# Performance work log

Hardware: AMD Instinct MI355X
Metric: run time of the kernel (lower is better)

The kernel has to match this reference:

```python
import jax, jax.numpy as jnp
import numpy as np

DIM = 384
NUM_HEADS = 12
HEAD_DIM = DIM // NUM_HEADS  # 32
SCALE = HEAD_DIM ** -0.5
B, N = 4, 2048


def setup_inputs() -> dict:
    key = jax.random.key(0)
    k0, k1, k2, k3 = jax.random.split(key, 4)
    x = jax.random.normal(k0, (B, N, DIM), dtype=jnp.float32)
    # nn.Linear(dim, 3*dim, bias=False): y = x @ W_qkv, W_qkv is [C, 3C]
    W_qkv = jax.random.normal(k1, (DIM, 3 * DIM), dtype=jnp.float32) * (DIM ** -0.5)
    # nn.Linear(dim, dim): y = x @ W_proj + b_proj, W_proj is [C, C]
    W_proj = jax.random.normal(k2, (DIM, DIM), dtype=jnp.float32) * (DIM ** -0.5)
    b_proj = jax.random.normal(k3, (DIM,), dtype=jnp.float32) * 0.01
    return {"x": x, "W_qkv": W_qkv, "W_proj": W_proj, "b_proj": b_proj}


def reference(x, W_qkv, W_proj, b_proj):
    b, n, c = x.shape
    qkv = (x @ W_qkv).reshape(b, n, 3, NUM_HEADS, HEAD_DIM)
    qkv = jnp.transpose(qkv, (2, 0, 3, 1, 4))  # [3, B, H, N, hd]
    q, k, v = qkv[0], qkv[1], qkv[2]
    # full attention: softmax(q k^T * scale) v
    attn = jnp.einsum('bhqd,bhkd->bhqk', q, k) * SCALE  # [B,H,N,N]
    attn = jax.nn.softmax(attn, axis=-1)
    out = jnp.einsum('bhqk,bhkd->bhqd', attn, v)  # [B,H,N,hd]
    out = jnp.transpose(out, (0, 2, 1, 3)).reshape(b, n, c)
    return out @ W_proj + b_proj
```

## Files before the change

kernel.cpp:

```cpp
#include <hip/hip_runtime.h>

constexpr int BB  = 4;
constexpr int SEQ = 2048;
constexpr int CC  = 384;
constexpr int C3  = 1152;
constexpr int NH  = 12;
constexpr int HD  = 32;
constexpr float SCALE = 0.17677669529663689f;
constexpr float LOG2E = 1.4426950408889634f;
constexpr float KSC   = SCALE * LOG2E;
constexpr size_t KV_BYTES = (size_t)2 * BB * NH * SEQ * HD * 2;
constexpr size_t WT_BYTES = ((size_t)C3 * CC + (size_t)CC * CC) * 2;
constexpr size_t XB_BYTES = (size_t)BB * SEQ * CC * 2;

typedef __attribute__((ext_vector_type(8))) short short8_t;
typedef __attribute__((ext_vector_type(4))) float floatx4;

#if __has_builtin(__builtin_amdgcn_exp2f)
#define EXP2F __builtin_amdgcn_exp2f
#else
#define EXP2F __builtin_exp2f
#endif

__device__ __forceinline__ unsigned short f2bf(float f) {
    unsigned int u = __builtin_bit_cast(unsigned int, f);
    u += 0x7fffu + ((u >> 16) & 1u);
    return (unsigned short)(u >> 16);
}
__device__ __forceinline__ unsigned int pk_rn(float lo, float hi) {
    return __builtin_amdgcn_perm(__builtin_bit_cast(unsigned int, hi) + 0x8000u,
                                 __builtin_bit_cast(unsigned int, lo) + 0x8000u,
                                 0x07060302u);
}
__device__ __forceinline__ unsigned int cvtpk(float lo, float hi) {
    unsigned int r;
    asm("v_cvt_pk_bf16_f32 %0, %1, %2" : "=v"(r) : "v"(lo), "v"(hi));
    return r;
}
__device__ __forceinline__ short8_t pack8(float4 a, float4 b) {
    uint4 u;
    u.x = pk_rn(a.x, a.y); u.y = pk_rn(a.z, a.w);
    u.z = pk_rn(b.x, b.y); u.w = pk_rn(b.z, b.w);
    return __builtin_bit_cast(short8_t, u);
}

__device__ __forceinline__ void vstore(unsigned short* vb, short8_t a, short8_t b) {
    const uint4 ua = __builtin_bit_cast(uint4, a);
    const uint4 ub = __builtin_bit_cast(uint4, b);
    *(uint2*)(vb)      = (uint2){ua.x, ua.y};
    *(uint2*)(vb + 8)  = (uint2){ua.z, ua.w};
    *(uint2*)(vb + 16) = (uint2){ub.x, ub.y};
    *(uint2*)(vb + 24) = (uint2){ub.z, ub.w};
}

__global__ __launch_bounds__(256) void prep_kernel(
    const float* __restrict__ x, const float* __restrict__ wqkv,
    const float* __restrict__ wproj,
    unsigned short* __restrict__ wqkvT, unsigned short* __restrict__ wprojT,
    unsigned short* __restrict__ xb)
{
    const int bid = blockIdx.x;
    if (bid >= 144) {
        const size_t base = (size_t)(bid - 144) * 2048 + threadIdx.x * 8;
        const float4 a = *(const float4*)(x + base);
        const float4 b = *(const float4*)(x + base + 4);
        uint4 u;
        u.x = pk_rn(a.x, a.y); u.y = pk_rn(a.z, a.w);
        u.z = pk_rn(b.x, b.y); u.w = pk_rn(b.z, b.w);
        *(uint4*)(xb + base) = u;
        return;
    }
    __shared__ float ls[64][68];
    const float* src; unsigned short* dst; int SN, k0, n0;
    if (bid < 108) {
        src = wqkv; dst = wqkvT; SN = C3;
        k0 = (bid / 18) * 64; n0 = (bid % 18) * 64;
    } else {
        const int b2 = bid - 108;
        src = wproj; dst = wprojT; SN = CC;
        k0 = (b2 / 6) * 64; n0 = (b2 % 6) * 64;
    }
    const int t  = threadIdx.x;
    const int rr = t >> 4, cc4 = (t & 15) * 4;
#pragma unroll
    for (int p = 0; p < 4; ++p) {
        const int row = p * 16 + rr;
        const float4 v = *(const float4*)&src[(size_t)(k0 + row) * SN + n0 + cc4];
        ls[row][cc4] = v.x; ls[row][cc4 + 1] = v.y;
        ls[row][cc4 + 2] = v.z; ls[row][cc4 + 3] = v.w;
    }
    __syncthreads();
#pragma unroll
    for (int p = 0; p < 4; ++p) {
        const int nrow = p * 16 + rr;
        uint2 u;
        u.x = pk_rn(ls[cc4][nrow],     ls[cc4 + 1][nrow]);
        u.y = pk_rn(ls[cc4 + 2][nrow], ls[cc4 + 3][nrow]);
        *(uint2*)&dst[(size_t)(n0 + nrow) * CC + k0 + cc4] = u;
    }
}

__global__ __launch_bounds__(256) void qkv_fast(
    const unsigned short* __restrict__ xb,
    const unsigned short* __restrict__ wT,
    unsigned short* __restrict__ qb,
    unsigned short* __restrict__ kv)
{
    __shared__ __align__(16) unsigned short As[2][128][40];
    __shared__ __align__(16) unsigned short Bs[2][128][40];

    const int mt   = blockIdx.x & 63;
    const int nb   = blockIdx.x >> 6;
    const int tid  = threadIdx.x;
    const int wid  = tid >> 6;
    const int lane = tid & 63;
    const int quad = lane >> 4;
    const int col  = lane & 15;
    const int wr   = wid >> 1, wc = wid & 1;
    const int m0 = mt * 128, n0 = nb * 128;

    const int arow = tid >> 1;
    const int aoff = (tid & 1) * 16;

    floatx4 acc[4][4];
#pragma unroll
    for (int i = 0; i < 4; ++i)
#pragma unroll
        for (int j = 0; j < 4; ++j) acc[i][j] = (floatx4){0.f, 0.f, 0.f, 0.f};

    const unsigned short* xrow = xb + (size_t)(m0 + arow) * CC + aoff;
    const unsigned short* wrow = wT + (size_t)(n0 + arow) * CC + aoff;

    short8_t ast0, ast1, bst0, bst1;
    ast0 = *(const short8_t*)xrow;
    ast1 = *(const short8_t*)(xrow + 8);
    bst0 = *(const short8_t*)wrow;
    bst1 = *(const short8_t*)(wrow + 8);
    *(short8_t*)&As[0][arow][aoff]     = ast0;
    *(short8_t*)&As[0][arow][aoff + 8] = ast1;
    *(short8_t*)&Bs[0][arow][aoff]     = bst0;
    *(short8_t*)&Bs[0][arow][aoff + 8] = bst1;

    for (int it = 0; it < CC / 32; ++it) {
        const int kn = (it + 1 < CC / 32) ? (it + 1) * 32 : 0;
        ast0 = *(const short8_t*)(xrow + kn);
        ast1 = *(const short8_t*)(xrow + kn + 8);
        bst0 = *(const short8_t*)(wrow + kn);
        bst1 = *(const short8_t*)(wrow + kn + 8);

        __syncthreads();
        const int p = it & 1;
        short8_t af[4], bf[4];
#pragma unroll
        for (int i = 0; i < 4; ++i)
            af[i] = *(const short8_t*)&As[p][wr * 64 + i * 16 + col][quad * 8];
#pragma unroll
        for (int j = 0; j < 4; ++j)
            bf[j] = *(const short8_t*)&Bs[p][wc * 64 + j * 16 + col][quad * 8];
#pragma unroll
        for (int j = 0; j < 4; ++j)
#pragma unroll
            for (int i = 0; i < 4; ++i)
                acc[i][j] = __builtin_amdgcn_mfma_f32_16x16x32_bf16(af[i], bf[j], acc[i][j], 0, 0, 0);

        *(short8_t*)&As[p ^ 1][arow][aoff]     = ast0;
        *(short8_t*)&As[p ^ 1][arow][aoff + 8] = ast1;
        *(short8_t*)&Bs[p ^ 1][arow][aoff]     = bst0;
        *(short8_t*)&Bs[p ^ 1][arow][aoff + 8] = bst1;
    }

    const int t = nb / 3;
#pragma unroll
    for (int i = 0; i < 4; ++i) {
        const int mg = m0 + wr * 64 + i * 16 + quad * 4;
        if (t == 0) {
#pragma unroll
            for (int j = 0; j < 4; ++j) {
                const int n = n0 + wc * 64 + j * 16 + col;
#pragma unroll
                for (int r = 0; r < 4; ++r)
                    qb[(size_t)(mg + r) * CC + n] = f2bf(acc[i][j][r]);
            }
        } else if (t == 1) {
            const int b = mg >> 11, s = mg & (SEQ - 1);
#pragma unroll
            for (int j = 0; j < 4; ++j) {
                const int rem = n0 - CC + wc * 64 + j * 16 + col;
                const int h = rem >> 5, d = rem & 31;
                unsigned short* kp = kv + ((size_t)(b * NH + h) * SEQ + s) * HD + d;
#pragma unroll
                for (int r = 0; r < 4; ++r)
                    kp[(size_t)r * HD] = f2bf(acc[i][j][r] * KSC);
            }
        } else {
            const int b = mg >> 11, s = mg & (SEQ - 1);
            unsigned short* vtb = kv + (size_t)BB * NH * SEQ * HD;
#pragma unroll
            for (int j = 0; j < 4; ++j) {
                const int rem = n0 - 2 * CC + wc * 64 + j * 16 + col;
                const int h = rem >> 5, d = rem & 31;
                uint2 u;
                u.x = pk_rn(acc[i][j][0], acc[i][j][1]);
                u.y = pk_rn(acc[i][j][2], acc[i][j][3]);
                *(uint2*)&vtb[((size_t)(b * NH + h) * HD + d) * SEQ + s] = u;
            }
        }
    }
}

__global__ __launch_bounds__(256, 3) void attn_kernel(
    const unsigned short* __restrict__ kv,
    const unsigned short* __restrict__ qb,
    unsigned short* __restrict__ ab)
{
    const int bid  = blockIdx.x;
    const int qp   = bid / 48;
    const int bh   = bid % 48;
    const int h    = bh % NH;
    const int b    = bh / NH;
    const int w    = threadIdx.x >> 6;
    const int lane = threadIdx.x & 63;
    const int quad = lane >> 4;
    const int col  = lane & 15;
    const int tid  = threadIdx.x;

    const unsigned short* K  = kv + (size_t)bh * SEQ * HD;
    const unsigned short* VT = kv + (size_t)BB * NH * SEQ * HD + (size_t)bh * HD * SEQ;

    __shared__ __align__(16) unsigned short Vt[2][32][136];

    const int drow_s = tid >> 3, voff_s = (tid & 7) * 16;
    const int vbase  = ((tid & 6) >> 1) * 32 + (tid & 1) * 4;

    const unsigned short* Kf = K + (size_t)col * HD + quad * 8;

    int qrow[2];
    short8_t qf[2];
#pragma unroll
    for (int t = 0; t < 2; ++t) {
        qrow[t] = b * SEQ + qp * 128 + (w + 4 * t) * 16 + col;
        qf[t] = *(const short8_t*)(qb + (size_t)qrow[t] * CC + h * HD + quad * 8);
    }

    short8_t ones;
#pragma unroll
    for (int e = 0; e < 8; ++e) ones[e] = (short)0x3F80;

    floatx4 o[2][2];
    floatx4 lacc[2];
#pragma unroll
    for (int t = 0; t < 2; ++t) {
        lacc[t] = (floatx4){0.f, 0.f, 0.f, 0.f};
#pragma unroll
        for (int i = 0; i < 2; ++i) o[t][i] = (floatx4){0.f, 0.f, 0.f, 0.f};
    }
    const float ci = -10.f * LOG2E;
    const floatx4 cinit = {ci, ci, ci, ci};

    short8_t v0a = *(const short8_t*)(VT + (size_t)drow_s * SEQ + voff_s);
    short8_t v0b = *(const short8_t*)(VT + (size_t)drow_s * SEQ + voff_s + 8);
    vstore(&Vt[0][drow_s][vbase], v0a, v0b);

    short8_t kaf[4][2];
#pragma unroll
    for (int c = 0; c < 4; ++c) {
        kaf[c][0] = *(const short8_t*)(Kf + (size_t)(c * 32) * HD);
        kaf[c][1] = *(const short8_t*)(Kf + (size_t)(c * 32 + 16) * HD);
    }

    for (int it = 0; it < SEQ / 128; ++it) {
        const int kn = ((it + 1) * 128) & (SEQ - 1);
        v0a = *(const short8_t*)(VT + (size_t)drow_s * SEQ + kn + voff_s);
        v0b = *(const short8_t*)(VT + (size_t)drow_s * SEQ + kn + voff_s + 8);
        const unsigned short* Kn = Kf + (size_t)kn * HD;

        __syncthreads();
        const int p = it & 1;

        short8_t va[4][2];
#pragma unroll
        for (int c = 0; c < 4; ++c) {
            const int c32 = c * 32;
            va[c][0] = *(const short8_t*)&Vt[p][col][c32 + quad * 8];
            va[c][1] = *(const short8_t*)&Vt[p][16 + col][c32 + quad * 8];
        }

#pragma unroll
        for (int c = 0; c < 4; ++c) {
            floatx4 s0[2], s1[2];
            __builtin_amdgcn_s_setprio(1);
#pragma unroll
            for (int t = 0; t < 2; ++t) {
                s0[t] = __builtin_amdgcn_mfma_f32_16x16x32_bf16(kaf[c][0], qf[t], cinit, 0, 0, 0);
                s1[t] = __builtin_amdgcn_mfma_f32_16x16x32_bf16(kaf[c][1], qf[t], cinit, 0, 0, 0);
            }
            __builtin_amdgcn_s_setprio(0);
            kaf[c][0] = *(const short8_t*)(Kn + (size_t)(c * 32) * HD);
            kaf[c][1] = *(const short8_t*)(Kn + (size_t)(c * 32 + 16) * HD);

            short8_t pb[2];
#pragma unroll
            for (int t = 0; t < 2; ++t) {
                const float p00 = EXP2F(s0[t][0]), p01 = EXP2F(s0[t][1]);
                const float p02 = EXP2F(s0[t][2]), p03 = EXP2F(s0[t][3]);
                const float p10 = EXP2F(s1[t][0]), p11 = EXP2F(s1[t][1]);
                const float p12 = EXP2F(s1[t][2]), p13 = EXP2F(s1[t][3]);
                const uint4 pu = {cvtpk(p00, p01), cvtpk(p02, p03),
                                  cvtpk(p10, p11), cvtpk(p12, p13)};
                pb[t] = __builtin_bit_cast(short8_t, pu);
            }
            __builtin_amdgcn_s_setprio(1);
#pragma unroll
            for (int t = 0; t < 2; ++t) {
                o[t][0] = __builtin_amdgcn_mfma_f32_16x16x32_bf16(va[c][0], pb[t], o[t][0], 0, 0, 0);
                o[t][1] = __builtin_amdgcn_mfma_f32_16x16x32_bf16(va[c][1], pb[t], o[t][1], 0, 0, 0);
                lacc[t] = __builtin_amdgcn_mfma_f32_16x16x32_bf16(ones, pb[t], lacc[t], 0, 0, 0);
            }
            __builtin_amdgcn_s_setprio(0);
        }

        vstore(&Vt[p ^ 1][drow_s][vbase], v0a, v0b);
    }

#pragma unroll
    for (int t = 0; t < 2; ++t) {
        const float inv = 1.f / lacc[t][0];
        unsigned short* op = ab + (size_t)qrow[t] * CC + h * HD;
#pragma unroll
        for (int i = 0; i < 2; ++i) {
            uint2 u;
            u.x = pk_rn(o[t][i][0] * inv, o[t][i][1] * inv);
            u.y = pk_rn(o[t][i][2] * inv, o[t][i][3] * inv);
            *(uint2*)&op[i * 16 + quad * 4] = u;
        }
    }
}

__global__ __launch_bounds__(256) void proj_fast(
    const unsigned short* __restrict__ ab,
    const unsigned short* __restrict__ wT,
    const float* __restrict__ bias,
    float* __restrict__ out)
{
    __shared__ __align__(16) unsigned short Bs[2][384][32];

    const int mt   = blockIdx.x;
    const int tid  = threadIdx.x;
    const int wid  = tid >> 6;
    const int lane = tid & 63;
    const int quad = lane >> 4;
    const int col  = lane & 15;
    const int m0   = mt * 32;

    floatx4 acc[2][6];
#pragma unroll
    for (int i = 0; i < 2; ++i)
#pragma unroll
        for (int j = 0; j < 6; ++j) acc[i][j] = (floatx4){0.f, 0.f, 0.f, 0.f};

    const unsigned short* arow0 = ab + (size_t)(m0 + col) * CC + quad * 8;
    const unsigned short* arow1 = arow0 + (size_t)16 * CC;

    short8_t bst[3][2];
    short8_t af0, af1;
    {
#pragma unroll
        for (int j = 0; j < 3; ++j) {
            const int f = j * 256 + tid;
            const unsigned short* wp = wT + (size_t)(f >> 1) * CC + (f & 1) * 16;
            bst[j][0] = *(const short8_t*)wp;
            bst[j][1] = *(const short8_t*)(wp + 8);
        }
        af0 = *(const short8_t*)arow0;
        af1 = *(const short8_t*)arow1;
#pragma unroll
        for (int j = 0; j < 3; ++j) {
            const int f = j * 256 + tid;
            *(short8_t*)&Bs[0][f >> 1][(f & 1) * 16]     = bst[j][0];
            *(short8_t*)&Bs[0][f >> 1][(f & 1) * 16 + 8] = bst[j][1];
        }
    }

    for (int it = 0; it < CC / 32; ++it) {
        const int kn = (it + 1 < CC / 32) ? (it + 1) * 32 : 0;
#pragma unroll
        for (int j = 0; j < 3; ++j) {
            const int f = j * 256 + tid;
            const unsigned short* wp = wT + (size_t)(f >> 1) * CC + kn + (f & 1) * 16;
            bst[j][0] = *(const short8_t*)wp;
            bst[j][1] = *(const short8_t*)(wp + 8);
        }
        const short8_t afn0 = *(const short8_t*)(arow0 + kn);
        const short8_t afn1 = *(const short8_t*)(arow1 + kn);

        __syncthreads();
        const int p = it & 1;
        short8_t bf[6];
#pragma unroll
        for (int j = 0; j < 6; ++j)
            bf[j] = *(const short8_t*)&Bs[p][wid * 96 + j * 16 + col][quad * 8];
#pragma unroll
        for (int j = 0; j < 6; ++j) {
            acc[0][j] = __builtin_amdgcn_mfma_f32_16x16x32_bf16(af0, bf[j], acc[0][j], 0, 0, 0);
            acc[1][j] = __builtin_amdgcn_mfma_f32_16x16x32_bf16(af1, bf[j], acc[1][j], 0, 0, 0);
        }

#pragma unroll
        for (int j = 0; j < 3; ++j) {
            const int f = j * 256 + tid;
            *(short8_t*)&Bs[p ^ 1][f >> 1][(f & 1) * 16]     = bst[j][0];
            *(short8_t*)&Bs[p ^ 1][f >> 1][(f & 1) * 16 + 8] = bst[j][1];
        }
        af0 = afn0; af1 = afn1;
    }

#pragma unroll
    for (int j = 0; j < 6; ++j) {
        const int n = wid * 96 + j * 16 + col;
        const float bv = bias[n];
#pragma unroll
        for (int i = 0; i < 2; ++i)
#pragma unroll
            for (int r = 0; r < 4; ++r)
                out[(size_t)(m0 + i * 16 + quad * 4 + r) * CC + n] = acc[i][j][r] + bv;
    }
}

__global__ __launch_bounds__(256) void qkv_lds(
    const float* __restrict__ x, const float* __restrict__ w,
    float* __restrict__ dq, unsigned short* __restrict__ kv)
{
    __shared__ __align__(16) unsigned short wt[128 * 40];
    const int mt = blockIdx.x & 63, nb = blockIdx.x >> 6;
    const int tid = threadIdx.x, wid = tid >> 6, lane = tid & 63;
    const int quad = lane >> 4, col = lane & 15;
    const int wr = wid >> 1, wc = wid & 1;
    const int m0 = mt * 128, n0 = nb * 128;
    const int sn = tid >> 1, skg = (tid & 1) * 4;

    floatx4 acc[4][4];
#pragma unroll
    for (int i = 0; i < 4; ++i)
#pragma unroll
        for (int j = 0; j < 4; ++j) acc[i][j] = (floatx4){0.f, 0.f, 0.f, 0.f};
    const float* xbase = x + (size_t)(m0 + wr * 64 + col) * CC;

    for (int kb = 0; kb < CC; kb += 32) {
        float wv[4][4];
#pragma unroll
        for (int s = 0; s < 4; ++s) {
            const int k = kb + (skg + s) * 4;
#pragma unroll
            for (int j = 0; j < 4; ++j) wv[s][j] = w[(size_t)(k + j) * C3 + n0 + sn];
        }
        short8_t af[4];
#pragma unroll
        for (int i = 0; i < 4; ++i) {
            const float* xr = xbase + (size_t)i * 16 * CC + kb + quad * 8;
            af[i] = pack8(*(const float4*)xr, *(const float4*)(xr + 4));
        }
        __syncthreads();
#pragma unroll
        for (int s = 0; s < 4; ++s) {
            ushort4 u;
            u.x = f2bf(wv[s][0]); u.y = f2bf(wv[s][1]);
            u.z = f2bf(wv[s][2]); u.w = f2bf(wv[s][3]);
            *(ushort4*)&wt[sn * 40 + (skg + s) * 4] = u;
        }
        __syncthreads();
#pragma unroll
        for (int j = 0; j < 4; ++j) {
            const short8_t bf = *(const short8_t*)&wt[(wc * 64 + j * 16 + col) * 40 + quad * 8];
#pragma unroll
            for (int i = 0; i < 4; ++i)
                acc[i][j] = __builtin_amdgcn_mfma_f32_16x16x32_bf16(af[i], bf, acc[i][j], 0, 0, 0);
        }
    }
    const int t = nb / 3;
#pragma unroll
    for (int i = 0; i < 4; ++i) {
        const int mg = m0 + wr * 64 + i * 16 + quad * 4;
        if (t == 0) {
#pragma unroll
            for (int j = 0; j < 4; ++j) {
                const int n = n0 + wc * 64 + j * 16 + col;
#pragma unroll
                for (int r = 0; r < 4; ++r) dq[(size_t)(mg + r) * CC + n] = acc[i][j][r];
            }
        } else if (t == 1) {
            const int b = mg >> 11, s = mg & (SEQ - 1);
#pragma unroll
            for (int j = 0; j < 4; ++j) {
                const int rem = n0 - CC + wc * 64 + j * 16 + col;
                const int h = rem >> 5, d = rem & 31;
                unsigned short* kp = kv + ((size_t)(b * NH + h) * SEQ + s) * HD + d;
#pragma unroll
                for (int r = 0; r < 4; ++r) kp[(size_t)r * HD] = f2bf(acc[i][j][r]);
            }
        } else {
            const int b = mg >> 11, s = mg & (SEQ - 1);
            unsigned short* vtb = kv + (size_t)BB * NH * SEQ * HD;
#pragma unroll
            for (int j = 0; j < 4; ++j) {
                const int rem = n0 - 2 * CC + wc * 64 + j * 16 + col;
                const int h = rem >> 5, d = rem & 31;
                uint2 u;
                u.x = pk_rn(acc[i][j][0], acc[i][j][1]);
                u.y = pk_rn(acc[i][j][2], acc[i][j][3]);
                *(uint2*)&vtb[((size_t)(b * NH + h) * HD + d) * SEQ + s] = u;
            }
        }
    }
}

__global__ __launch_bounds__(256) void attn_f32(
    const unsigned short* __restrict__ kv,
    float* qatt)
{
    const int bid  = blockIdx.x;
    const int qp   = bid / 48;
    const int bh   = bid % 48;
    const int h    = bh % NH;
    const int b    = bh / NH;
    const int w    = threadIdx.x >> 6;
    const int lane = threadIdx.x & 63;
    const int quad = lane >> 4;
    const int col  = lane & 15;
    const int tid  = threadIdx.x;

    const unsigned short* K  = kv + (size_t)bh * SEQ * HD;
    const unsigned short* VT = kv + (size_t)BB * NH * SEQ * HD + (size_t)bh * HD * SEQ;

    __shared__ __align__(16) unsigned short Kt[2][128][40];
    __shared__ __align__(16) unsigned short Vt[2][32][136];

    const int krow_s = tid >> 1, koff_s = (tid & 1) * 16;
    const int drow_s = tid >> 3, voff_s = (tid & 7) * 16;

    int qrow[2];
    short8_t qf[2];
    const float sc = SCALE * LOG2E;
#pragma unroll
    for (int t = 0; t < 2; ++t) {
        qrow[t] = b * SEQ + qp * 128 + (w + 4 * t) * 16 + col;
        const float* qpt = qatt + (size_t)qrow[t] * CC + h * HD + quad * 8;
        const float4 a0 = *(const float4*)qpt;
        const float4 a1 = *(const float4*)(qpt + 4);
        const float4 s0 = {a0.x * sc, a0.y * sc, a0.z * sc, a0.w * sc};
        const float4 s1 = {a1.x * sc, a1.y * sc, a1.z * sc, a1.w * sc};
        qf[t] = pack8(s0, s1);
    }

    short8_t ones;
#pragma unroll
    for (int e = 0; e < 8; ++e) ones[e] = (short)0x3F80;

    floatx4 o[2][2];
    floatx4 lacc[2];
#pragma unroll
    for (int t = 0; t < 2; ++t) {
        lacc[t] = (floatx4){0.f, 0.f, 0.f, 0.f};
#pragma unroll
        for (int i = 0; i < 2; ++i) o[t][i] = (floatx4){0.f, 0.f, 0.f, 0.f};
    }
    const float ci = -10.f * LOG2E;
    const floatx4 cinit = {ci, ci, ci, ci};

    short8_t k0a = *(const short8_t*)(K + (size_t)krow_s * HD + koff_s);
    short8_t k0b = *(const short8_t*)(K + (size_t)krow_s * HD + koff_s + 8);
    short8_t v0a = *(const short8_t*)(VT + (size_t)drow_s * SEQ + voff_s);
    short8_t v0b = *(const short8_t*)(VT + (size_t)drow_s * SEQ + voff_s + 8);
    *(short8_t*)&Kt[0][krow_s][koff_s]     = k0a;
    *(short8_t*)&Kt[0][krow_s][koff_s + 8] = k0b;
    *(short8_t*)&Vt[0][drow_s][voff_s]     = v0a;
    *(short8_t*)&Vt[0][drow_s][voff_s + 8] = v0b;

    for (int it = 0; it < SEQ / 128; ++it) {
        const int kn = ((it + 1) * 128) & (SEQ - 1);
        k0a = *(const short8_t*)(K + (size_t)(kn + krow_s) * HD + koff_s);
        k0b = *(const short8_t*)(K + (size_t)(kn + krow_s) * HD + koff_s + 8);
        v0a = *(const short8_t*)(VT + (size_t)drow_s * SEQ + kn + voff_s);
        v0b = *(const short8_t*)(VT + (size_t)drow_s * SEQ + kn + voff_s + 8);

        __syncthreads();
        const int p = it & 1;

#pragma unroll
        for (int c = 0; c < 4; ++c) {
            const int c32 = c * 32;
            const short8_t ka0 = *(const short8_t*)&Kt[p][c32 + col][quad * 8];
            const short8_t ka1 = *(const short8_t*)&Kt[p][c32 + 16 + col][quad * 8];
            const uint2 w0a = *(const uint2*)&Vt[p][col][c32 + quad * 4];
            const uint2 w0b = *(const uint2*)&Vt[p][col][c32 + 16 + quad * 4];
            const uint2 w1a = *(const uint2*)&Vt[p][16 + col][c32 + quad * 4];
            const uint2 w1b = *(const uint2*)&Vt[p][16 + col][c32 + 16 + quad * 4];
            const short8_t va0 = __builtin_bit_cast(short8_t, (uint4){w0a.x, w0a.y, w0b.x, w0b.y});
            const short8_t va1 = __builtin_bit_cast(short8_t, (uint4){w1a.x, w1a.y, w1b.x, w1b.y});
#pragma unroll
            for (int t = 0; t < 2; ++t) {
                const floatx4 s0 = __builtin_amdgcn_mfma_f32_16x16x32_bf16(ka0, qf[t], cinit, 0, 0, 0);
                const floatx4 s1 = __builtin_amdgcn_mfma_f32_16x16x32_bf16(ka1, qf[t], cinit, 0, 0, 0);
                const float p00 = EXP2F(s0[0]), p01 = EXP2F(s0[1]);
                const float p02 = EXP2F(s0[2]), p03 = EXP2F(s0[3]);
                const float p10 = EXP2F(s1[0]), p11 = EXP2F(s1[1]);
                const float p12 = EXP2F(s1[2]), p13 = EXP2F(s1[3]);
                const uint4 pu = {pk_rn(p00, p01), pk_rn(p02, p03),
                                  pk_rn(p10, p11), pk_rn(p12, p13)};
                const short8_t pb = __builtin_bit_cast(short8_t, pu);
                o[t][0] = __builtin_amdgcn_mfma_f32_16x16x32_bf16(va0, pb, o[t][0], 0, 0, 0);
                o[t][1] = __builtin_amdgcn_mfma_f32_16x16x32_bf16(va1, pb, o[t][1], 0, 0, 0);
                lacc[t] = __builtin_amdgcn_mfma_f32_16x16x32_bf16(ones, pb, lacc[t], 0, 0, 0);
            }
        }

        *(short8_t*)&Kt[p ^ 1][krow_s][koff_s]     = k0a;
        *(short8_t*)&Kt[p ^ 1][krow_s][koff_s + 8] = k0b;
        *(short8_t*)&Vt[p ^ 1][drow_s][voff_s]     = v0a;
        *(short8_t*)&Vt[p ^ 1][drow_s][voff_s + 8] = v0b;
    }

#pragma unroll
    for (int t = 0; t < 2; ++t) {
        const float inv = 1.f / lacc[t][0];
        float* op = qatt + (size_t)qrow[t] * CC + h * HD;
#pragma unroll
        for (int r = 0; r < 4; ++r) {
            op[quad * 4 + r]      = o[t][0][r] * inv;
            op[16 + quad * 4 + r] = o[t][1][r] * inv;
        }
    }
}

__global__ __launch_bounds__(256) void proj_lds(
    float* att, const float* __restrict__ wp, const float* __restrict__ bias)
{
    __shared__ __align__(16) unsigned short wt[CC * 40];
    const int mt = blockIdx.x, tid = threadIdx.x, wid = tid >> 6, lane = tid & 63;
    const int quad = lane >> 4, col = lane & 15;
    const int m0 = mt * 16;
    floatx4 acc[6];
#pragma unroll
    for (int j = 0; j < 6; ++j) acc[j] = (floatx4){0.f, 0.f, 0.f, 0.f};
    for (int kb = 0; kb < CC; kb += 32) {
        float gv[12][4];
#pragma unroll
        for (int g = 0; g < 12; ++g) {
            const int flat = tid + g * 256, n = flat % 384, kg = flat / 384;
#pragma unroll
            for (int j = 0; j < 4; ++j) gv[g][j] = wp[(size_t)(kb + kg * 4 + j) * CC + n];
        }
        __syncthreads();
#pragma unroll
        for (int g = 0; g < 12; ++g) {
            const int flat = tid + g * 256, n = flat % 384, kg = flat / 384;
            ushort4 u;
            u.x = f2bf(gv[g][0]); u.y = f2bf(gv[g][1]);
            u.z = f2bf(gv[g][2]); u.w = f2bf(gv[g][3]);
            *(ushort4*)&wt[n * 40 + kg * 4] = u;
        }
        __syncthreads();
        const float* ap = att + (size_t)(m0 + col) * CC + kb + quad * 8;
        const short8_t af = pack8(*(const float4*)ap, *(const float4*)(ap + 4));
#pragma unroll
        for (int j = 0; j < 6; ++j) {
            const short8_t pb = *(const short8_t*)&wt[(wid * 96 + j * 16 + col) * 40 + quad * 8];
            acc[j] = __builtin_amdgcn_mfma_f32_16x16x32_bf16(af, pb, acc[j], 0, 0, 0);
        }
    }
    __syncthreads();
#pragma unroll
    for (int j = 0; j < 6; ++j) {
        const int n = wid * 96 + j * 16 + col;
        const float bv = bias[n];
#pragma unroll
        for (int r = 0; r < 4; ++r)
            att[(size_t)(m0 + quad * 4 + r) * CC + n] = acc[j][r] + bv;
    }
}

__global__ void marker_kernel(float* out, float val, int nelem) {
    int i = blockIdx.x * 256 + threadIdx.x;
    if (i < nelem) out[i] = val;
}

extern "C" void kernel_launch(void* const* d_in, const int* in_sizes, int n_in,
                              void* d_out, int out_size, void* d_ws, size_t ws_size,
                              hipStream_t stream)
{
    const float* x     = (const float*)d_in[0];
    const float* wqkv  = (const float*)d_in[1];
    const float* wproj = (const float*)d_in[2];
    const float* bproj = (const float*)d_in[3];
    float* out = (float*)d_out;
    unsigned short* kv = (unsigned short*)d_ws;

    if (ws_size < KV_BYTES) {
        const float marker = 100.f + (float)(ws_size >> 20);
        marker_kernel<<<(out_size + 255) / 256, 256, 0, stream>>>(out, marker, out_size);
        return;
    }

    unsigned short* wqkvT  = kv + (size_t)2 * BB * NH * SEQ * HD;
    unsigned short* wprojT = wqkvT + (size_t)C3 * CC;
    unsigned short* xb     = wprojT + (size_t)CC * CC;

    if (ws_size >= KV_BYTES + WT_BYTES + XB_BYTES) {
        unsigned short* qb = (unsigned short*)d_out;
        prep_kernel<<<144 + 1536, 256, 0, stream>>>(x, wqkv, wproj, wqkvT, wprojT, xb);
        qkv_fast<<<576, 256, 0, stream>>>(xb, wqkvT, qb, kv);
        attn_kernel<<<16 * BB * NH, 256, 0, stream>>>(kv, qb, xb );
        proj_fast<<<BB * SEQ / 32, 256, 0, stream>>>(xb, wprojT, bproj, out);
    } else {
        qkv_lds<<<576, 256, 0, stream>>>(x, wqkv, out, kv);
        attn_f32<<<16 * BB * NH, 256, 0, stream>>>(kv, out);
        proj_lds<<<BB * SEQ / 16, 256, 0, stream>>>(out, wproj, bproj);
    }
}
```

Measured before the change: 133.3 us.

## Halve attention query tile per block and split proj across 8 waves

The attention kernel now gives each wave one 16-row query tile instead of two, so each block covers 64 queries, and the grid doubles to 1536 blocks with a higher occupancy hint in launch bounds. The projection kernel moves to 512 threads, with waves split over M and N so each wave handles one 16-row A fragment. The aim is more parallelism and occupancy and lower register pressure. The cost is that every K/V tile is loaded and staged through LDS twice as often per query, and the MFMA work between loads is halved.

```diff
diff --git a/kernel.cpp b/kernel.cpp
--- a/kernel.cpp
+++ b/kernel.cpp
@@ -208,7 +208,7 @@
     }
 }
 
-__global__ __launch_bounds__(256, 3) void attn_kernel(
+__global__ __launch_bounds__(256, 4) void attn_kernel(
     const unsigned short* __restrict__ kv,
     const unsigned short* __restrict__ qb,
     unsigned short* __restrict__ ab)
@@ -234,26 +234,17 @@
 
     const unsigned short* Kf = K + (size_t)col * HD + quad * 8;
 
-    int qrow[2];
-    short8_t qf[2];
-#pragma unroll
-    for (int t = 0; t < 2; ++t) {
-        qrow[t] = b * SEQ + qp * 128 + (w + 4 * t) * 16 + col;
-        qf[t] = *(const short8_t*)(qb + (size_t)qrow[t] * CC + h * HD + quad * 8);
-    }
+    const int qrow = b * SEQ + qp * 64 + w * 16 + col;
+    const short8_t qf = *(const short8_t*)(qb + (size_t)qrow * CC + h * HD + quad * 8);
 
     short8_t ones;
 #pragma unroll
     for (int e = 0; e < 8; ++e) ones[e] = (short)0x3F80;
 
-    floatx4 o[2][2];
-    floatx4 lacc[2];
-#pragma unroll
-    for (int t = 0; t < 2; ++t) {
-        lacc[t] = (floatx4){0.f, 0.f, 0.f, 0.f};
-#pragma unroll
-        for (int i = 0; i < 2; ++i) o[t][i] = (floatx4){0.f, 0.f, 0.f, 0.f};
-    }
+    floatx4 o[2];
+    floatx4 lacc = (floatx4){0.f, 0.f, 0.f, 0.f};
+    o[0] = (floatx4){0.f, 0.f, 0.f, 0.f};
+    o[1] = (floatx4){0.f, 0.f, 0.f, 0.f};
     const float ci = -10.f * LOG2E;
     const floatx4 cinit = {ci, ci, ci, ci};
 
@@ -287,56 +278,42 @@
 
 #pragma unroll
         for (int c = 0; c < 4; ++c) {
-            floatx4 s0[2], s1[2];
             __builtin_amdgcn_s_setprio(1);
-#pragma unroll
-            for (int t = 0; t < 2; ++t) {
-                s0[t] = __builtin_amdgcn_mfma_f32_16x16x32_bf16(kaf[c][0], qf[t], cinit, 0, 0, 0);
-                s1[t] = __builtin_amdgcn_mfma_f32_16x16x32_bf16(kaf[c][1], qf[t], cinit, 0, 0, 0);
-            }
+            const floatx4 s0 = __builtin_amdgcn_mfma_f32_16x16x32_bf16(kaf[c][0], qf, cinit, 0, 0, 0);
+            const floatx4 s1 = __builtin_amdgcn_mfma_f32_16x16x32_bf16(kaf[c][1], qf, cinit, 0, 0, 0);
             __builtin_amdgcn_s_setprio(0);
             kaf[c][0] = *(const short8_t*)(Kn + (size_t)(c * 32) * HD);
             kaf[c][1] = *(const short8_t*)(Kn + (size_t)(c * 32 + 16) * HD);
 
-            short8_t pb[2];
-#pragma unroll
-            for (int t = 0; t < 2; ++t) {
-                const float p00 = EXP2F(s0[t][0]), p01 = EXP2F(s0[t][1]);
-                const float p02 = EXP2F(s0[t][2]), p03 = EXP2F(s0[t][3]);
-                const float p10 = EXP2F(s1[t][0]), p11 = EXP2F(s1[t][1]);
-                const float p12 = EXP2F(s1[t][2]), p13 = EXP2F(s1[t][3]);
-                const uint4 pu = {cvtpk(p00, p01), cvtpk(p02, p03),
-                                  cvtpk(p10, p11), cvtpk(p12, p13)};
-                pb[t] = __builtin_bit_cast(short8_t, pu);
-            }
+            const float p00 = EXP2F(s0[0]), p01 = EXP2F(s0[1]);
+            const float p02 = EXP2F(s0[2]), p03 = EXP2F(s0[3]);
+            const float p10 = EXP2F(s1[0]), p11 = EXP2F(s1[1]);
+            const float p12 = EXP2F(s1[2]), p13 = EXP2F(s1[3]);
+            const uint4 pu = {cvtpk(p00, p01), cvtpk(p02, p03),
+                              cvtpk(p10, p11), cvtpk(p12, p13)};
+            const short8_t pb = __builtin_bit_cast(short8_t, pu);
             __builtin_amdgcn_s_setprio(1);
-#pragma unroll
-            for (int t = 0; t < 2; ++t) {
-                o[t][0] = __builtin_amdgcn_mfma_f32_16x16x32_bf16(va[c][0], pb[t], o[t][0], 0, 0, 0);
-                o[t][1] = __builtin_amdgcn_mfma_f32_16x16x32_bf16(va[c][1], pb[t], o[t][1], 0, 0, 0);
-                lacc[t] = __builtin_amdgcn_mfma_f32_16x16x32_bf16(ones, pb[t], lacc[t], 0, 0, 0);
-            }
+            o[0] = __builtin_amdgcn_mfma_f32_16x16x32_bf16(va[c][0], pb, o[0], 0, 0, 0);
+            o[1] = __builtin_amdgcn_mfma_f32_16x16x32_bf16(va[c][1], pb, o[1], 0, 0, 0);
+            lacc = __builtin_amdgcn_mfma_f32_16x16x32_bf16(ones, pb, lacc, 0, 0, 0);
             __builtin_amdgcn_s_setprio(0);
         }
 
         vstore(&Vt[p ^ 1][drow_s][vbase], v0a, v0b);
     }
 
-#pragma unroll
-    for (int t = 0; t < 2; ++t) {
-        const float inv = 1.f / lacc[t][0];
-        unsigned short* op = ab + (size_t)qrow[t] * CC + h * HD;
-#pragma unroll
-        for (int i = 0; i < 2; ++i) {
-            uint2 u;
-            u.x = pk_rn(o[t][i][0] * inv, o[t][i][1] * inv);
-            u.y = pk_rn(o[t][i][2] * inv, o[t][i][3] * inv);
-            *(uint2*)&op[i * 16 + quad * 4] = u;
-        }
-    }
-}
-
-__global__ __launch_bounds__(256) void proj_fast(
+    const float inv = 1.f / lacc[0];
+    unsigned short* op = ab + (size_t)qrow * CC + h * HD;
+#pragma unroll
+    for (int i = 0; i < 2; ++i) {
+        uint2 u;
+        u.x = pk_rn(o[i][0] * inv, o[i][1] * inv);
+        u.y = pk_rn(o[i][2] * inv, o[i][3] * inv);
+        *(uint2*)&op[i * 16 + quad * 4] = u;
+    }
+}
+
+__global__ __launch_bounds__(512) void proj_fast(
     const unsigned short* __restrict__ ab,
     const unsigned short* __restrict__ wT,
     const float* __restrict__ bias,
@@ -347,82 +324,79 @@
     const int mt   = blockIdx.x;
     const int tid  = threadIdx.x;
     const int wid  = tid >> 6;
+    const int wn   = wid & 3;
+    const int wm   = wid >> 2;
     const int lane = tid & 63;
     const int quad = lane >> 4;
     const int col  = lane & 15;
     const int m0   = mt * 32;
 
-    floatx4 acc[2][6];
-#pragma unroll
-    for (int i = 0; i < 2; ++i)
-#pragma unroll
-        for (int j = 0; j < 6; ++j) acc[i][j] = (floatx4){0.f, 0.f, 0.f, 0.f};
-
-    const unsigned short* arow0 = ab + (size_t)(m0 + col) * CC + quad * 8;
-    const unsigned short* arow1 = arow0 + (size_t)16 * CC;
-
-    short8_t bst[3][2];
-    short8_t af0, af1;
+    floatx4 acc[6];
+#pragma unroll
+    for (int j = 0; j < 6; ++j) acc[j] = (floatx4){0.f, 0.f, 0.f, 0.f};
+
+    const unsigned short* arow = ab + (size_t)(m0 + wm * 16 + col) * CC + quad * 8;
+
+    const int f1 = tid;
+    const int f2 = 512 + tid;
+    const bool has2 = tid < 256;
+    const unsigned short* wp1 = wT + (size_t)(f1 >> 1) * CC + (f1 & 1) * 16;
+    const unsigned short* wp2 = wT + (size_t)(f2 >> 1) * CC + (f2 & 1) * 16;
+
+    short8_t bA0, bA1, bB0, bB1;
+    short8_t af;
     {
-#pragma unroll
-        for (int j = 0; j < 3; ++j) {
-            const int f = j * 256 + tid;
-            const unsigned short* wp = wT + (size_t)(f >> 1) * CC + (f & 1) * 16;
-            bst[j][0] = *(const short8_t*)wp;
-            bst[j][1] = *(const short8_t*)(wp + 8);
-        }
-        af0 = *(const short8_t*)arow0;
-        af1 = *(const short8_t*)arow1;
-#pragma unroll
-        for (int j = 0; j < 3; ++j) {
-            const int f = j * 256 + tid;
-            *(short8_t*)&Bs[0][f >> 1][(f & 1) * 16]     = bst[j][0];
-            *(short8_t*)&Bs[0][f >> 1][(f & 1) * 16 + 8] = bst[j][1];
+        bA0 = *(const short8_t*)wp1;
+        bA1 = *(const short8_t*)(wp1 + 8);
+        if (has2) {
+            bB0 = *(const short8_t*)wp2;
+            bB1 = *(const short8_t*)(wp2 + 8);
+        }
+        af = *(const short8_t*)arow;
+        *(short8_t*)&Bs[0][f1 >> 1][(f1 & 1) * 16]     = bA0;
+        *(short8_t*)&Bs[0][f1 >> 1][(f1 & 1) * 16 + 8] = bA1;
+        if (has2) {
+            *(short8_t*)&Bs[0][f2 >> 1][(f2 & 1) * 16]     = bB0;
+            *(short8_t*)&Bs[0][f2 >> 1][(f2 & 1) * 16 + 8] = bB1;
         }
     }
 
     for (int it = 0; it < CC / 32; ++it) {
         const int kn = (it + 1 < CC / 32) ? (it + 1) * 32 : 0;
-#pragma unroll
-        for (int j = 0; j < 3; ++j) {
-            const int f = j * 256 + tid;
-            const unsigned short* wp = wT + (size_t)(f >> 1) * CC + kn + (f & 1) * 16;
-            bst[j][0] = *(const short8_t*)wp;
-            bst[j][1] = *(const short8_t*)(wp + 8);
-        }
-        const short8_t afn0 = *(const short8_t*)(arow0 + kn);
-        const short8_t afn1 = *(const short8_t*)(arow1 + kn);
+        bA0 = *(const short8_t*)(wp1 + kn);
+        bA1 = *(const short8_t*)(wp1 + kn + 8);
+        if (has2) {
+            bB0 = *(const short8_t*)(wp2 + kn);
+            bB1 = *(const short8_t*)(wp2 + kn + 8);
+        }
+        const short8_t afn = *(const short8_t*)(arow + kn);
 
         __syncthreads();
         const int p = it & 1;
         short8_t bf[6];
 #pragma unroll
         for (int j = 0; j < 6; ++j)
-            bf[j] = *(const short8_t*)&Bs[p][wid * 96 + j * 16 + col][quad * 8];
-#pragma unroll
-        for (int j = 0; j < 6; ++j) {
-            acc[0][j] = __builtin_amdgcn_mfma_f32_16x16x32_bf16(af0, bf[j], acc[0][j], 0, 0, 0);
-            acc[1][j] = __builtin_amdgcn_mfma_f32_16x16x32_bf16(af1, bf[j], acc[1][j], 0, 0, 0);
-        }
-
-#pragma unroll
-        for (int j = 0; j < 3; ++j) {
-            const int f = j * 256 + tid;
-            *(short8_t*)&Bs[p ^ 1][f >> 1][(f & 1) * 16]     = bst[j][0];
-            *(short8_t*)&Bs[p ^ 1][f >> 1][(f & 1) * 16 + 8] = bst[j][1];
-        }
-        af0 = afn0; af1 = afn1;
+            bf[j] = *(const short8_t*)&Bs[p][wn * 96 + j * 16 + col][quad * 8];
+#pragma unroll
+        for (int j = 0; j < 6; ++j)
+            acc[j] = __builtin_amdgcn_mfma_f32_16x16x32_bf16(af, bf[j], acc[j], 0, 0, 0);
+
+        *(short8_t*)&Bs[p ^ 1][f1 >> 1][(f1 & 1) * 16]     = bA0;
+        *(short8_t*)&Bs[p ^ 1][f1 >> 1][(f1 & 1) * 16 + 8] = bA1;
+        if (has2) {
+            *(short8_t*)&Bs[p ^ 1][f2 >> 1][(f2 & 1) * 16]     = bB0;
+            *(short8_t*)&Bs[p ^ 1][f2 >> 1][(f2 & 1) * 16 + 8] = bB1;
+        }
+        af = afn;
     }
 
 #pragma unroll
     for (int j = 0; j < 6; ++j) {
-        const int n = wid * 96 + j * 16 + col;
+        const int n = wn * 96 + j * 16 + col;
         const float bv = bias[n];
 #pragma unroll
-        for (int i = 0; i < 2; ++i)
-#pragma unroll
-            for (int r = 0; r < 4; ++r)
-                out[(size_t)(m0 + i * 16 + quad * 4 + r) * CC + n] = acc[i][j][r] + bv;
+        for (int r = 0; r < 4; ++r)
+            out[(size_t)(m0 + wm * 16 + quad * 4 + r) * CC + n] = acc[j][r] + bv;
     }
 }
 
@@ -708,8 +682,8 @@
         unsigned short* qb = (unsigned short*)d_out;
         prep_kernel<<<144 + 1536, 256, 0, stream>>>(x, wqkv, wproj, wqkvT, wprojT, xb);
         qkv_fast<<<576, 256, 0, stream>>>(xb, wqkvT, qb, kv);
-        attn_kernel<<<16 * BB * NH, 256, 0, stream>>>(kv, qb, xb );
-        proj_fast<<<BB * SEQ / 32, 256, 0, stream>>>(xb, wprojT, bproj, out);
+        attn_kernel<<<32 * BB * NH, 256, 0, stream>>>(kv, qb, xb );
+        proj_fast<<<BB * SEQ / 32, 512, 0, stream>>>(xb, wprojT, bproj, out);
     } else {
         qkv_lds<<<576, 256, 0, stream>>>(x, wqkv, out, kv);
         attn_f32<<<16 * BB * NH, 256, 0, stream>>>(kv, out);
```

Result: slower. 152.3 us (+14.2%).
